# Optimization experiments

Hardware: AMD Instinct MI355X
Metric: run time of the kernel (lower is better)

## Reference

```python
import jax, jax.numpy as jnp
import numpy as np
import math
from jax import lax


def quick_gelu(v):
    return v * jax.nn.sigmoid(1.702 * v)


def setup_inputs() -> dict:
    key = jax.random.key(0)
    k0, k1, k2, k3 = jax.random.split(key, 4)
    B, N, C, dim = 64, 1024, 768, 8
    x = jax.random.normal(k0, (B, N, C), dtype=jnp.float32)
    # adapter_down: Linear(C -> dim), xavier-ish init
    Wd = jax.random.normal(k1, (C, dim), dtype=jnp.float32) * (1.0 / math.sqrt(C))
    bd = jnp.zeros((dim,), dtype=jnp.float32)
    # adapter_conv: Conv2d(dim, dim, 3, stride=1, pad=1), HWIO layout
    Wc = jax.random.normal(k2, (3, 3, dim, dim), dtype=jnp.float32) * (1.0 / math.sqrt(9 * dim))
    bc = jnp.zeros((dim,), dtype=jnp.float32)
    # adapter_up: Linear(dim -> C); torch inits this to zeros, but use small
    # random values so the output/gradients are non-trivial for testing.
    Wu = jax.random.normal(k3, (dim, C), dtype=jnp.float32) * 0.02
    bu = jnp.zeros((C,), dtype=jnp.float32)
    return {"x": x, "Wd": Wd, "bd": bd, "Wc": Wc, "bc": bc, "Wu": Wu, "bu": bu}


def reference(x, Wd, bd, Wc, bc, Wu, bu):
    B, N, C = x.shape
    H = int(math.isqrt(N))  # N is a static perfect square (patch grid)
    dim = Wd.shape[1]
    # down projection: [B, N, C] -> [B, N, dim]
    x_down = jnp.einsum("bnc,cd->bnd", x, Wd) + bd
    # reshape to NHWC patch grid, activate, 3x3 same-pad conv
    x_patch = quick_gelu(x_down.reshape(B, H, H, dim))
    x_patch = lax.conv_general_dilated(
        x_patch, Wc, window_strides=(1, 1), padding="SAME",
        dimension_numbers=("NHWC", "HWIO", "NHWC")) + bc
    # flatten back, activate (dropout = identity in eval), up projection
    x_down = quick_gelu(x_patch.reshape(B, N, dim))
    x_up = jnp.einsum("bnd,dc->bnc", x_down, Wu) + bu
    return x_up
```

## Files before the change

### kernel.cpp

```cpp
#include <hip/hip_runtime.h>

#define B_  64
#define N_  1024
#define H_  32
#define C_  768
#define D_  8

#define QCHUNKS   4
#define IMG_PER_Q (B_ / QCHUNKS)
#define ROWS_PER_Q (IMG_PER_Q * N_)
#define NDOWN     512
#define NUP       (IMG_PER_Q * 4)

__device__ __forceinline__ float qgelu(float v) {
    return v / (1.0f + __expf(-1.702f * v));
}

typedef float f32x4_t __attribute__((ext_vector_type(4)));
__device__ __forceinline__ float4 ntload4(const float4* p) {
    f32x4_t v = __builtin_nontemporal_load((const f32x4_t*)p);
    return make_float4(v.x, v.y, v.z, v.w);
}
__device__ __forceinline__ void ntstore4(float4 v, float4* p) {
    f32x4_t t; t.x = v.x; t.y = v.y; t.z = v.z; t.w = v.w;
    __builtin_nontemporal_store(t, (f32x4_t*)p);
}

__device__ __forceinline__ void reduce8(float* acc, int lane) {
    {
        const bool hi = lane & 1;
#pragma unroll
        for (int j = 0; j < 4; ++j) {
            const float a = acc[j], b = acc[j + 4];
            acc[j] = hi ? b : a;
            acc[j + 4] = hi ? a : b;
        }
#pragma unroll
        for (int j = 0; j < 4; ++j)
            acc[j] += __shfl_xor(acc[j + 4], 1, 64);
    }
    {
        const bool hi = lane & 2;
#pragma unroll
        for (int j = 0; j < 2; ++j) {
            const float a = acc[j], b = acc[j + 2];
            acc[j] = hi ? b : a;
            acc[j + 2] = hi ? a : b;
        }
#pragma unroll
        for (int j = 0; j < 2; ++j)
            acc[j] += __shfl_xor(acc[j + 2], 2, 64);
    }
    {
        const bool hi = lane & 4;
        const float a = acc[0], b = acc[1];
        acc[0] = hi ? b : a;
        acc[1] = hi ? a : b;
        acc[0] += __shfl_xor(acc[1], 4, 64);
    }
    acc[0] += __shfl_xor(acc[0], 8, 64);
    acc[0] += __shfl_xor(acc[0], 16, 64);
    acc[0] += __shfl_xor(acc[0], 32, 64);
}

__global__ __launch_bounds__(256) void k_step(
    const float* __restrict__ x,  const float* __restrict__ Wd,
    const float* __restrict__ bd, float* __restrict__ t1,
    const float* __restrict__ Wc, const float* __restrict__ bc,
    const float* __restrict__ Wu, const float* __restrict__ bu,
    float* __restrict__ out, int downBase, int nDown, int upImg0)
{
    __shared__ float smem[D_ * C_];

    const int wid  = threadIdx.x >> 6;
    const int lane = threadIdx.x & 63;

    if ((int)blockIdx.x < nDown) {
        float* sW = smem;
        for (int i = threadIdx.x; i < D_ * C_; i += 256) {
            const int c = i >> 3, d = i & 7;
            sW[d * C_ + c] = Wd[i];
        }
        __syncthreads();

        const int dl = 4 * (lane & 1) + 2 * ((lane >> 1) & 1) + ((lane >> 2) & 1);
        const float bias = bd[dl];
        const int pairBase = (downBase >> 1) + blockIdx.x * 16 + wid * 4;

#pragma unroll 1
        for (int i = 0; i < 4; ++i) {
            const int p = pairBase + i;
            const float4* x0 = (const float4*)(x + (size_t)(2 * p) * C_);
            const float4* x1 = x0 + (C_ / 4);

            float4 va[3], vb[3];
#pragma unroll
            for (int k = 0; k < 3; ++k) {
                va[k] = ntload4(&x0[k * 64 + lane]);
                vb[k] = ntload4(&x1[k * 64 + lane]);
            }

            float a0[D_], a1[D_];
#pragma unroll
            for (int d = 0; d < D_; ++d) { a0[d] = 0.0f; a1[d] = 0.0f; }

#pragma unroll
            for (int k = 0; k < 3; ++k) {
#pragma unroll
                for (int d = 0; d < D_; ++d) {
                    const float4 wv = *(const float4*)&sW[d * C_ + (k * 64 + lane) * 4];
                    a0[d] += va[k].x * wv.x + va[k].y * wv.y
                           + va[k].z * wv.z + va[k].w * wv.w;
                    a1[d] += vb[k].x * wv.x + vb[k].y * wv.y
                           + vb[k].z * wv.z + vb[k].w * wv.w;
                }
            }

            reduce8(a0, lane);
            reduce8(a1, lane);

            if (lane < 16) {
                const float s = (lane & 8) ? a1[0] : a0[0];
                t1[(size_t)(2 * p + ((lane >> 3) & 1)) * D_ + dl] = qgelu(s + bias);
            }
        }
    } else {
        float* sIn = smem;
        float* sT2 = smem + 2560;
        float* sWc = smem + 4608;
        float* sbc = smem + 5184;

        const int idx   = blockIdx.x - nDown;
        const int img   = upImg0 + (idx >> 2);
        const int strip = idx & 3;
        const int h0    = strip * 8;
        const float* in = t1 + (size_t)img * N_ * D_;

#pragma unroll
        for (int j = 0; j < 10; ++j) {
            const int i   = threadIdx.x + j * 256;
            const int lr  = i >> 8;
            const int rem = i & 255;
            const int g   = h0 - 1 + lr;
            sIn[i] = (g >= 0 && g < H_) ? in[(size_t)g * H_ * D_ + rem] : 0.0f;
        }
        for (int i = threadIdx.x; i < 9 * D_ * D_; i += 256) sWc[i] = Wc[i];
        if (threadIdx.x < D_) sbc[threadIdx.x] = bc[threadIdx.x];

        float4 wu[3][D_];
        float4 ub[3];
#pragma unroll
        for (int j = 0; j < 3; ++j) {
            ub[j] = *(const float4*)&bu[(lane + j * 64) * 4];
#pragma unroll
            for (int d = 0; d < D_; ++d)
                wu[j][d] = *(const float4*)&Wu[d * C_ + (lane + j * 64) * 4];
        }
        __syncthreads();

        {
            const int lh = threadIdx.x >> 5;
            const int w  = threadIdx.x & 31;
            float acc[D_];
#pragma unroll
            for (int co = 0; co < D_; ++co) acc[co] = sbc[co];
#pragma unroll
            for (int kh = 0; kh < 3; ++kh) {
                const int lrow = lh + kh;
#pragma unroll
                for (int kw = 0; kw < 3; ++kw) {
                    const int ww = w + kw - 1;
                    if (ww < 0 || ww >= H_) continue;
                    const float* ip = &sIn[(lrow * H_ + ww) * D_];
                    const float* wp = &sWc[(kh * 3 + kw) * D_ * D_];
#pragma unroll
                    for (int ci = 0; ci < D_; ++ci) {
                        const float iv = ip[ci];
#pragma unroll
                        for (int co = 0; co < D_; ++co)
                            acc[co] += iv * wp[ci * D_ + co];
                    }
                }
            }
            float* tp = &sT2[(lh * H_ + w) * D_];
#pragma unroll
            for (int co = 0; co < D_; ++co) tp[co] = qgelu(acc[co]);
        }
        __syncthreads();

        const size_t rowBase = (size_t)img * N_ + strip * 256;
#pragma unroll 1
        for (int r = 0; r < 64; ++r) {
            const int  row = wid * 64 + r;
            const float* tv = &sT2[row * D_];
            float rv[D_];
#pragma unroll
            for (int d = 0; d < D_; ++d) rv[d] = tv[d];

            float* orow = out + (rowBase + row) * C_;
#pragma unroll
            for (int j = 0; j < 3; ++j) {
                float4 o = ub[j];
#pragma unroll
                for (int d = 0; d < D_; ++d) {
                    o.x += rv[d] * wu[j][d].x;
                    o.y += rv[d] * wu[j][d].y;
                    o.z += rv[d] * wu[j][d].z;
                    o.w += rv[d] * wu[j][d].w;
                }
                ntstore4(o, (float4*)&orow[(lane + j * 64) * 4]);
            }
        }
    }
}

extern "C" void kernel_launch(void* const* d_in, const int* in_sizes, int n_in,
                              void* d_out, int out_size, void* d_ws, size_t ws_size,
                              hipStream_t stream) {
    const float* x  = (const float*)d_in[0];
    const float* Wd = (const float*)d_in[1];
    const float* bd = (const float*)d_in[2];
    const float* Wc = (const float*)d_in[3];
    const float* bc = (const float*)d_in[4];
    const float* Wu = (const float*)d_in[5];
    const float* bu = (const float*)d_in[6];
    float* out = (float*)d_out;

    float* t1 = (float*)d_ws;

    for (int s = 0; s <= QCHUNKS; ++s) {
        const int nDown  = (s < QCHUNKS) ? NDOWN : 0;
        const int nUp    = (s > 0) ? NUP : 0;
        const int grid   = nDown + nUp;
        const int dBase  = s * ROWS_PER_Q;
        const int uImg0  = (s - 1) * IMG_PER_Q;
        k_step<<<grid, 256, 0, stream>>>(x, Wd, bd, t1, Wc, bc, Wu, bu, out,
                                         dBase, nDown, uImg0);
    }
}
```

Measured before the change: 108.5 us.

## Split conv and up-projection into separate pipeline stages across launches

Turns the two-stage chunked pipeline (down, then conv+up) into a three-stage one. Conv results now go to a global t2 buffer, and a separate up-projection stage with 256 blocks per chunk reads them and writes the output. Before, only 64 conv+up blocks per chunk did the dominant output write. The change aims to spread the heavy output store across many more blocks and to overlap it with the down and conv work of later chunks. In exchange it adds one more launch, a global round trip for t2, and Wu staged through LDS instead of registers.

```diff
diff --git a/kernel.cpp b/kernel.cpp
--- a/kernel.cpp
+++ b/kernel.cpp
@@ -6,11 +6,12 @@
 #define C_  768
 #define D_  8
 
-#define QCHUNKS   4
-#define IMG_PER_Q (B_ / QCHUNKS)
+#define QCHUNKS    4
+#define IMG_PER_Q  (B_ / QCHUNKS)
 #define ROWS_PER_Q (IMG_PER_Q * N_)
-#define NDOWN     512
-#define NUP       (IMG_PER_Q * 4)
+#define NDOWN      512
+#define NCONV      (IMG_PER_Q * 4)
+#define NUPB       256
 
 __device__ __forceinline__ float qgelu(float v) {
     return v / (1.0f + __expf(-1.702f * v));
@@ -67,15 +68,57 @@
     const float* __restrict__ x,  const float* __restrict__ Wd,
     const float* __restrict__ bd, float* __restrict__ t1,
     const float* __restrict__ Wc, const float* __restrict__ bc,
-    const float* __restrict__ Wu, const float* __restrict__ bu,
-    float* __restrict__ out, int downBase, int nDown, int upImg0)
+    float* __restrict__ t2,       const float* __restrict__ Wu,
+    const float* __restrict__ bu, float* __restrict__ out,
+    int nUp, int upC, int nDown, int downC, int nConv, int convC)
 {
     __shared__ float smem[D_ * C_];
-
     const int wid  = threadIdx.x >> 6;
     const int lane = threadIdx.x & 63;
-
-    if ((int)blockIdx.x < nDown) {
+    const int bid  = blockIdx.x;
+
+    if (bid < nUp) {
+        float* sW = smem;
+        for (int i = threadIdx.x; i < D_ * C_; i += 256) sW[i] = Wu[i];
+        __syncthreads();
+
+        float4 ub[3];
+#pragma unroll
+        for (int j = 0; j < 3; ++j)
+            ub[j] = *(const float4*)&bu[(lane + j * 64) * 4];
+
+        const int rowBase = upC * ROWS_PER_Q + bid * 64 + wid * 16;
+#pragma unroll 1
+        for (int pr = 0; pr < 8; ++pr) {
+            const int row = rowBase + pr * 2;
+            const float4* rp = (const float4*)(t2 + (size_t)row * D_);
+            const float4 r0a = rp[0], r0b = rp[1];
+            const float4 r1a = rp[2], r1b = rp[3];
+            const float rv0[D_] = { r0a.x,r0a.y,r0a.z,r0a.w, r0b.x,r0b.y,r0b.z,r0b.w };
+            const float rv1[D_] = { r1a.x,r1a.y,r1a.z,r1a.w, r1b.x,r1b.y,r1b.z,r1b.w };
+
+            float4 o0[3], o1[3];
+#pragma unroll
+            for (int j = 0; j < 3; ++j) { o0[j] = ub[j]; o1[j] = ub[j]; }
+#pragma unroll
+            for (int d = 0; d < D_; ++d) {
+#pragma unroll
+                for (int j = 0; j < 3; ++j) {
+                    const float4 wv = *(const float4*)&sW[d * C_ + (lane + j * 64) * 4];
+                    o0[j].x += rv0[d] * wv.x; o0[j].y += rv0[d] * wv.y;
+                    o0[j].z += rv0[d] * wv.z; o0[j].w += rv0[d] * wv.w;
+                    o1[j].x += rv1[d] * wv.x; o1[j].y += rv1[d] * wv.y;
+                    o1[j].z += rv1[d] * wv.z; o1[j].w += rv1[d] * wv.w;
+                }
+            }
+            float* orow0 = out + (size_t)row * C_;
+#pragma unroll
+            for (int j = 0; j < 3; ++j) {
+                ntstore4(o0[j], (float4*)&orow0[(lane + j * 64) * 4]);
+                ntstore4(o1[j], (float4*)&orow0[C_ + (lane + j * 64) * 4]);
+            }
+        }
+    } else if (bid < nUp + nDown) {
         float* sW = smem;
         for (int i = threadIdx.x; i < D_ * C_; i += 256) {
             const int c = i >> 3, d = i & 7;
@@ -85,7 +128,7 @@
 
         const int dl = 4 * (lane & 1) + 2 * ((lane >> 1) & 1) + ((lane >> 2) & 1);
         const float bias = bd[dl];
-        const int pairBase = (downBase >> 1) + blockIdx.x * 16 + wid * 4;
+        const int pairBase = (downC * ROWS_PER_Q >> 1) + (bid - nUp) * 16 + wid * 4;
 
 #pragma unroll 1
         for (int i = 0; i < 4; ++i) {
@@ -115,10 +158,8 @@
                            + vb[k].z * wv.z + vb[k].w * wv.w;
                 }
             }
-
             reduce8(a0, lane);
             reduce8(a1, lane);
-
             if (lane < 16) {
                 const float s = (lane & 8) ? a1[0] : a0[0];
                 t1[(size_t)(2 * p + ((lane >> 3) & 1)) * D_ + dl] = qgelu(s + bias);
@@ -126,12 +167,11 @@
         }
     } else {
         float* sIn = smem;
-        float* sT2 = smem + 2560;
-        float* sWc = smem + 4608;
-        float* sbc = smem + 5184;
-
-        const int idx   = blockIdx.x - nDown;
-        const int img   = upImg0 + (idx >> 2);
+        float* sWc = smem + 2560;
+        float* sbc = smem + 3136;
+
+        const int idx   = bid - nUp - nDown;
+        const int img   = convC * IMG_PER_Q + (idx >> 2);
         const int strip = idx & 3;
         const int h0    = strip * 8;
         const float* in = t1 + (size_t)img * N_ * D_;
@@ -146,71 +186,39 @@
         }
         for (int i = threadIdx.x; i < 9 * D_ * D_; i += 256) sWc[i] = Wc[i];
         if (threadIdx.x < D_) sbc[threadIdx.x] = bc[threadIdx.x];
-
-        float4 wu[3][D_];
-        float4 ub[3];
-#pragma unroll
-        for (int j = 0; j < 3; ++j) {
-            ub[j] = *(const float4*)&bu[(lane + j * 64) * 4];
-#pragma unroll
-            for (int d = 0; d < D_; ++d)
-                wu[j][d] = *(const float4*)&Wu[d * C_ + (lane + j * 64) * 4];
-        }
         __syncthreads();
 
-        {
-            const int lh = threadIdx.x >> 5;
-            const int w  = threadIdx.x & 31;
-            float acc[D_];
-#pragma unroll
-            for (int co = 0; co < D_; ++co) acc[co] = sbc[co];
-#pragma unroll
-            for (int kh = 0; kh < 3; ++kh) {
-                const int lrow = lh + kh;
-#pragma unroll
-                for (int kw = 0; kw < 3; ++kw) {
-                    const int ww = w + kw - 1;
-                    if (ww < 0 || ww >= H_) continue;
-                    const float* ip = &sIn[(lrow * H_ + ww) * D_];
-                    const float* wp = &sWc[(kh * 3 + kw) * D_ * D_];
-#pragma unroll
-                    for (int ci = 0; ci < D_; ++ci) {
-                        const float iv = ip[ci];
-#pragma unroll
-                        for (int co = 0; co < D_; ++co)
-                            acc[co] += iv * wp[ci * D_ + co];
-                    }
+        const int lh = threadIdx.x >> 5;
+        const int w  = threadIdx.x & 31;
+        float acc[D_];
+#pragma unroll
+        for (int co = 0; co < D_; ++co) acc[co] = sbc[co];
+#pragma unroll
+        for (int kh = 0; kh < 3; ++kh) {
+            const int lrow = lh + kh;
+#pragma unroll
+            for (int kw = 0; kw < 3; ++kw) {
+                const int ww = w + kw - 1;
+                if (ww < 0 || ww >= H_) continue;
+                const float* ip = &sIn[(lrow * H_ + ww) * D_];
+                const float* wp = &sWc[(kh * 3 + kw) * D_ * D_];
+#pragma unroll
+                for (int ci = 0; ci < D_; ++ci) {
+                    const float iv = ip[ci];
+#pragma unroll
+                    for (int co = 0; co < D_; ++co)
+                        acc[co] += iv * wp[ci * D_ + co];
                 }
             }
-            float* tp = &sT2[(lh * H_ + w) * D_];
-#pragma unroll
-            for (int co = 0; co < D_; ++co) tp[co] = qgelu(acc[co]);
-        }
-        __syncthreads();
-
-        const size_t rowBase = (size_t)img * N_ + strip * 256;
-#pragma unroll 1
-        for (int r = 0; r < 64; ++r) {
-            const int  row = wid * 64 + r;
-            const float* tv = &sT2[row * D_];
-            float rv[D_];
-#pragma unroll
-            for (int d = 0; d < D_; ++d) rv[d] = tv[d];
-
-            float* orow = out + (rowBase + row) * C_;
-#pragma unroll
-            for (int j = 0; j < 3; ++j) {
-                float4 o = ub[j];
-#pragma unroll
-                for (int d = 0; d < D_; ++d) {
-                    o.x += rv[d] * wu[j][d].x;
-                    o.y += rv[d] * wu[j][d].y;
-                    o.z += rv[d] * wu[j][d].z;
-                    o.w += rv[d] * wu[j][d].w;
-                }
-                ntstore4(o, (float4*)&orow[(lane + j * 64) * 4]);
-            }
-        }
+        }
+        float4 o0, o1;
+        o0.x = qgelu(acc[0]); o0.y = qgelu(acc[1]);
+        o0.z = qgelu(acc[2]); o0.w = qgelu(acc[3]);
+        o1.x = qgelu(acc[4]); o1.y = qgelu(acc[5]);
+        o1.z = qgelu(acc[6]); o1.w = qgelu(acc[7]);
+        float* tp = t2 + ((size_t)img * N_ + (size_t)(h0 + lh) * H_ + w) * D_;
+        *(float4*)tp       = o0;
+        *(float4*)(tp + 4) = o1;
     }
 }
 
@@ -226,15 +234,16 @@
     const float* bu = (const float*)d_in[6];
     float* out = (float*)d_out;
 
+    const int nrows = B_ * N_;
     float* t1 = (float*)d_ws;
-
-    for (int s = 0; s <= QCHUNKS; ++s) {
-        const int nDown  = (s < QCHUNKS) ? NDOWN : 0;
-        const int nUp    = (s > 0) ? NUP : 0;
-        const int grid   = nDown + nUp;
-        const int dBase  = s * ROWS_PER_Q;
-        const int uImg0  = (s - 1) * IMG_PER_Q;
-        k_step<<<grid, 256, 0, stream>>>(x, Wd, bd, t1, Wc, bc, Wu, bu, out,
-                                         dBase, nDown, uImg0);
-    }
-}
+    float* t2 = t1 + (size_t)nrows * D_;
+
+    for (int s = 0; s < QCHUNKS + 2; ++s) {
+        const int nD = (s < QCHUNKS) ? NDOWN : 0;
+        const int nC = (s >= 1 && s <= QCHUNKS) ? NCONV : 0;
+        const int nU = (s >= 2) ? NUPB : 0;
+        k_step<<<nU + nD + nC, 256, 0, stream>>>(
+            x, Wd, bd, t1, Wc, bc, t2, Wu, bu, out,
+            nU, s - 2, nD, s, nC, s - 1);
+    }
+}
```

Result: slower. 113.9 us (+5.1%).
